# Kernel tuning notes

Hardware: AMD Instinct MI355X
Metric: run time of the kernel (lower is better)

The kernel has to match this reference:

```python
import jax, jax.numpy as jnp
import numpy as np

N = 50000      # nodes
E = 800000     # edges
F_IN = 128     # num_features
H = 64         # hidden_dim
G = 64         # graphs in batch
EPS = 1e-5


def setup_inputs() -> dict:
    ks = jax.random.split(jax.random.key(0), 16)
    x = jax.random.normal(ks[0], (N, F_IN), dtype=jnp.float32)
    edge_index = jax.random.randint(ks[1], (2, E), 0, N, dtype=jnp.int64)
    batch = jnp.sort(jax.random.randint(ks[2], (N,), 0, G, dtype=jnp.int64))
    s = 0.05
    inp = {"x": x, "edge_index": edge_index, "batch": batch}
    # GCNConv layers: W [out,in], bias [out]; BatchNorm gamma/beta [H]
    dims = [(H, F_IN), (H, H), (H, H)]
    for i, (o, ci) in enumerate(dims):
        inp[f"W{i}"] = jax.random.normal(ks[3 + i], (o, ci), dtype=jnp.float32) * s
        inp[f"b{i}"] = jnp.zeros((o,), dtype=jnp.float32)
        inp[f"g{i}"] = jnp.ones((o,), dtype=jnp.float32)
        inp[f"be{i}"] = jnp.zeros((o,), dtype=jnp.float32)
    inp["lin1_w"] = jax.random.normal(ks[10], (H // 2, H), dtype=jnp.float32) * s
    inp["lin1_b"] = jnp.zeros((H // 2,), dtype=jnp.float32)
    inp["lin2_w"] = jax.random.normal(ks[11], (1, H // 2), dtype=jnp.float32) * s
    inp["lin2_b"] = jnp.zeros((1,), dtype=jnp.float32)
    return inp


def _gcn_conv(x, src, dst, W, b):
    # PyG GCNConv: h = x W^T; add self-loops; symmetric deg^{-1/2} norm; scatter-add; + bias
    h = x @ W.T                                   # [N, out]
    n = x.shape[0]
    deg = jax.ops.segment_sum(jnp.ones(src.shape[0], h.dtype), dst, num_segments=n) + 1.0
    dinv = jax.lax.rsqrt(deg)                     # [N]
    msg = h[src] * (dinv[src] * dinv[dst])[:, None]   # per-edge messages
    agg = jax.ops.segment_sum(msg, dst, num_segments=n)
    agg = agg + h * (dinv * dinv)[:, None]        # self-loop contribution
    return agg + b


def _bn_relu(x, g, be):
    # BatchNorm1d (training-mode batch stats, biased var) + ReLU; dropout = identity (eval)
    m = x.mean(axis=0)
    v = jnp.var(x, axis=0)
    return jax.nn.relu((x - m) * jax.lax.rsqrt(v + EPS) * g + be)


def reference(x, edge_index, batch,
              W0, b0, g0, be0, W1, b1, g1, be1, W2, b2, g2, be2,
              lin1_w, lin1_b, lin2_w, lin2_b):
    src, dst = edge_index[0], edge_index[1]
    Ws = [(W0, b0, g0, be0), (W1, b1, g1, be1), (W2, b2, g2, be2)]
    h = x
    for (W, b, g, be) in Ws:
        h = _bn_relu(_gcn_conv(h, src, dst, W, b), g, be)
    # global mean pool over graphs
    sums = jax.ops.segment_sum(h, batch, num_segments=G)          # [G, H]
    cnt = jax.ops.segment_sum(jnp.ones((h.shape[0],), h.dtype), batch, num_segments=G)
    pooled = sums / jnp.maximum(cnt, 1.0)[:, None]
    h = jax.nn.relu(pooled @ lin1_w.T + lin1_b)
    return h @ lin2_w.T + lin2_b                                   # [G, 1]
```

## Files before the change

kernel.cpp:

```cpp
#include <hip/hip_runtime.h>

#define NN 50000
#define NE 800000
#define FIN 128
#define H 64
#define NG 64
#define BN_EPS 1e-5f
#define INV_N (1.0f / 50000.0f)
#define NBKT 196
#define PB 256
#define SLICE 64
#define BKCAP 8192
#define PROWS 16

__device__ __forceinline__ void f4acc(float4& a, const float4 b) {
    a.x += b.x; a.y += b.y; a.z += b.z; a.w += b.w;
}
__device__ __forceinline__ void f4accw(float4& a, const float4 b, float w) {
    a.x += b.x * w; a.y += b.y * w; a.z += b.z * w; a.w += b.w * w;
}

__global__ void prep(const float* __restrict__ W0, const float* __restrict__ W1,
                     const float* __restrict__ W2, const int* __restrict__ src,
                     const int* __restrict__ dst, float* __restrict__ Wt0,
                     float* __restrict__ Wt1, float* __restrict__ Wt2,
                     float* __restrict__ sl0, float* __restrict__ sl1,
                     float* __restrict__ sl2, float* __restrict__ pool,
                     float* __restrict__ cnt, int* __restrict__ done,
                     int* __restrict__ cnts, unsigned int* __restrict__ staged) {
    const int tid = threadIdx.x, bid = blockIdx.x;
    const int gtid = bid * 256 + tid;
    const int gsz = PB * 256;
    for (int i = gtid; i < 64 * 128; i += gsz) { sl0[i] = 0.f; sl1[i] = 0.f; sl2[i] = 0.f; }
    for (int i = gtid; i < NG * H; i += gsz) pool[i] = 0.f;
    if (gtid < NG) cnt[gtid] = 0.f;
    if (gtid == 0) *done = 0;
    for (int i = gtid; i < FIN * 64; i += gsz) {
        int k = i >> 6, o = i & 63;
        Wt0[i] = W0[o * FIN + k];
    }
    for (int i = gtid; i < H * 64; i += gsz) {
        int k = i >> 6, o = i & 63;
        Wt1[i] = W1[o * H + k];
        Wt2[i] = W2[o * H + k];
    }
    __shared__ int hcnt[NBKT];
    for (int i = tid; i < NBKT; i += 256) hcnt[i] = 0;
    __syncthreads();
    const int chunk = NE / PB;
    const int e0 = bid * chunk, e1 = e0 + chunk;
    for (int e = e0 + tid; e < e1; e += 256) {
        int d = dst[e];
        int s = src[e];
        int bkt = d >> 8;
        int idx = atomicAdd(&hcnt[bkt], 1);
        if (idx < SLICE)
            staged[(size_t)(bkt * PB + bid) * SLICE + idx] =
                (unsigned int)s | ((unsigned int)(d & 255) << 16);
    }
    __syncthreads();
    for (int i = tid; i < NBKT; i += 256) cnts[i * PB + bid] = min(hcnt[i], SLICE);
}

union CsrMmSh {
    struct { float Xs[64 * 68]; float Ws[64 * 64]; } mm;
    struct { int cnt[256]; int loc[256]; int cur[256]; int spre[257]; } csr;
};

__device__ __forceinline__ int slice_find(const int* __restrict__ spre, int t) {
    int lo = 0, hi = 255;
    while (lo < hi) {
        int mid = (lo + hi + 1) >> 1;
        if (spre[mid] <= t) lo = mid; else hi = mid - 1;
    }
    return lo;
}

template <int K>
__device__ __forceinline__ void mm_tile_body(int base, const float* __restrict__ x,
                                             const float* __restrict__ Wtg,
                                             const float* __restrict__ slots,
                                             const float* __restrict__ gamma,
                                             const float* __restrict__ beta,
                                             const float* __restrict__ dv,
                                             float* __restrict__ outp, float* Xs, float* Ws,
                                             float* st, int n) {
    const int tid = threadIdx.x;
    if (slots) {
        if (tid < 128) {
            float s0 = 0.f, s1 = 0.f, s2 = 0.f, s3 = 0.f;
            for (int k = 0; k < 64; k += 4) {
                s0 += slots[(k + 0) * 128 + tid];
                s1 += slots[(k + 1) * 128 + tid];
                s2 += slots[(k + 2) * 128 + tid];
                s3 += slots[(k + 3) * 128 + tid];
            }
            st[tid] = (s0 + s1) + (s2 + s3);
        }
        __syncthreads();
    }
    const int q = tid >> 4;
    const int co = (tid & 15) * 4;
    const int kq = (tid & 15) * 4;
    float4 a0 = make_float4(0.f, 0.f, 0.f, 0.f);
    float4 a1 = a0, a2 = a0, a3 = a0;

    for (int kc = 0; kc < K; kc += 64) {
        if (kc) __syncthreads();
        for (int i = tid; i < 64 * 64; i += 256) Ws[i] = Wtg[kc * 64 + i];
        {
            float4 sc = make_float4(1.f, 1.f, 1.f, 1.f);
            float4 sh = make_float4(0.f, 0.f, 0.f, 0.f);
            if (slots) {
                int kk = kc + kq;
                float4 s = *(const float4*)&st[kk];
                float4 ss = *(const float4*)&st[64 + kk];
                float4 gm = *(const float4*)&gamma[kk];
                float4 bt = *(const float4*)&beta[kk];
                float mx = s.x * INV_N, my = s.y * INV_N, mz = s.z * INV_N, mw = s.w * INV_N;
                sc.x = gm.x * rsqrtf(ss.x * INV_N - mx * mx + BN_EPS);
                sc.y = gm.y * rsqrtf(ss.y * INV_N - my * my + BN_EPS);
                sc.z = gm.z * rsqrtf(ss.z * INV_N - mz * mz + BN_EPS);
                sc.w = gm.w * rsqrtf(ss.w * INV_N - mw * mw + BN_EPS);
                sh.x = bt.x - mx * sc.x;
                sh.y = bt.y - my * sc.y;
                sh.z = bt.z - mz * sc.z;
                sh.w = bt.w - mw * sc.w;
            }
            for (int j = 0; j < 4; ++j) {
                int r = (tid >> 4) + j * 16;
                int row = base + r;
                float4 v = make_float4(0.f, 0.f, 0.f, 0.f);
                if (row < n) v = *(const float4*)&x[(size_t)row * K + kc + kq];
                if (slots) {
                    v.x = fmaxf(v.x * sc.x + sh.x, 0.f);
                    v.y = fmaxf(v.y * sc.y + sh.y, 0.f);
                    v.z = fmaxf(v.z * sc.z + sh.z, 0.f);
                    v.w = fmaxf(v.w * sc.w + sh.w, 0.f);
                }
                *(float4*)&Xs[r * 68 + kq] = v;
            }
        }
        __syncthreads();

#pragma unroll 2
        for (int k = 0; k < 64; k += 4) {
            float4 x0 = *(const float4*)&Xs[(q + 0) * 68 + k];
            float4 x1 = *(const float4*)&Xs[(q + 16) * 68 + k];
            float4 x2 = *(const float4*)&Xs[(q + 32) * 68 + k];
            float4 x3 = *(const float4*)&Xs[(q + 48) * 68 + k];
            float4 w0 = *(const float4*)&Ws[(k + 0) * 64 + co];
            float4 w1 = *(const float4*)&Ws[(k + 1) * 64 + co];
            float4 w2 = *(const float4*)&Ws[(k + 2) * 64 + co];
            float4 w3 = *(const float4*)&Ws[(k + 3) * 64 + co];

            a0.x += x0.x * w0.x + x0.y * w1.x + x0.z * w2.x + x0.w * w3.x;
            a0.y += x0.x * w0.y + x0.y * w1.y + x0.z * w2.y + x0.w * w3.y;
            a0.z += x0.x * w0.z + x0.y * w1.z + x0.z * w2.z + x0.w * w3.z;
            a0.w += x0.x * w0.w + x0.y * w1.w + x0.z * w2.w + x0.w * w3.w;

            a1.x += x1.x * w0.x + x1.y * w1.x + x1.z * w2.x + x1.w * w3.x;
            a1.y += x1.x * w0.y + x1.y * w1.y + x1.z * w2.y + x1.w * w3.y;
            a1.z += x1.x * w0.z + x1.y * w1.z + x1.z * w2.z + x1.w * w3.z;
            a1.w += x1.x * w0.w + x1.y * w1.w + x1.z * w2.w + x1.w * w3.w;

            a2.x += x2.x * w0.x + x2.y * w1.x + x2.z * w2.x + x2.w * w3.x;
            a2.y += x2.x * w0.y + x2.y * w1.y + x2.z * w2.y + x2.w * w3.y;
            a2.z += x2.x * w0.z + x2.y * w1.z + x2.z * w2.z + x2.w * w3.z;
            a2.w += x2.x * w0.w + x2.y * w1.w + x2.z * w2.w + x2.w * w3.w;

            a3.x += x3.x * w0.x + x3.y * w1.x + x3.z * w2.x + x3.w * w3.x;
            a3.y += x3.x * w0.y + x3.y * w1.y + x3.z * w2.y + x3.w * w3.y;
            a3.z += x3.x * w0.z + x3.y * w1.z + x3.z * w2.z + x3.w * w3.z;
            a3.w += x3.x * w0.w + x3.y * w1.w + x3.z * w2.w + x3.w * w3.w;
        }
    }

    int r0 = base + q;
    if (r0 < n) {
        float d = dv ? dv[r0] : 1.f;
        a0.x *= d; a0.y *= d; a0.z *= d; a0.w *= d;
        *(float4*)&outp[(size_t)r0 * H + co] = a0;
    }
    if (r0 + 16 < n) {
        float d = dv ? dv[r0 + 16] : 1.f;
        a1.x *= d; a1.y *= d; a1.z *= d; a1.w *= d;
        *(float4*)&outp[(size_t)(r0 + 16) * H + co] = a1;
    }
    if (r0 + 32 < n) {
        float d = dv ? dv[r0 + 32] : 1.f;
        a2.x *= d; a2.y *= d; a2.z *= d; a2.w *= d;
        *(float4*)&outp[(size_t)(r0 + 32) * H + co] = a2;
    }
    if (r0 + 48 < n) {
        float d = dv ? dv[r0 + 48] : 1.f;
        a3.x *= d; a3.y *= d; a3.z *= d; a3.w *= d;
        *(float4*)&outp[(size_t)(r0 + 48) * H + co] = a3;
    }
}

__global__ __launch_bounds__(256, 4) void csr_mm0(
    const unsigned int* __restrict__ staged, const int* __restrict__ cnts,
    int* __restrict__ rs, int* __restrict__ re, float* __restrict__ dinv,
    int* __restrict__ csr, const float* __restrict__ x, const float* __restrict__ Wt0,
    float* __restrict__ bufA) {
    __shared__ CsrMmSh sh;
    const int tid = threadIdx.x;
    if (blockIdx.x < NBKT) {
        const int b = blockIdx.x;
        int c = cnts[b * PB + tid];
        sh.csr.loc[tid] = c;
        sh.csr.cnt[tid] = 0;
        __syncthreads();
        for (int off = 1; off < 256; off <<= 1) {
            int t = (tid >= off) ? sh.csr.loc[tid - off] : 0;
            __syncthreads();
            sh.csr.loc[tid] += t;
            __syncthreads();
        }
        sh.csr.spre[tid] = sh.csr.loc[tid] - c;
        if (tid == 255) sh.csr.spre[256] = sh.csr.loc[255];
        __syncthreads();
        const int T = sh.csr.spre[256];
        for (int t = tid; t < T; t += 256) {
            int s = slice_find(sh.csr.spre, t);
            unsigned int u = staged[(size_t)(b * PB + s) * SLICE + (t - sh.csr.spre[s])];
            atomicAdd(&sh.csr.cnt[(u >> 16) & 255], 1);
        }
        __syncthreads();
        int v = sh.csr.cnt[tid];
        sh.csr.loc[tid] = v;
        __syncthreads();
        for (int off = 1; off < 256; off <<= 1) {
            int t = (tid >= off) ? sh.csr.loc[tid - off] : 0;
            __syncthreads();
            sh.csr.loc[tid] += t;
            __syncthreads();
        }
        const int start = b * BKCAP + sh.csr.loc[tid] - v;
        const int node = b * 256 + tid;
        if (node < NN) {
            rs[node] = start;
            re[node] = start + v;
            dinv[node] = rsqrtf((float)v + 1.0f);
        }
        sh.csr.cur[tid] = start;
        __syncthreads();
        for (int t = tid; t < T; t += 256) {
            int s = slice_find(sh.csr.spre, t);
            unsigned int u = staged[(size_t)(b * PB + s) * SLICE + (t - sh.csr.spre[s])];
            int j = atomicAdd(&sh.csr.cur[(u >> 16) & 255], 1);
            csr[j] = (int)(u & 0xFFFFu);
        }
    } else {
        mm_tile_body<FIN>((blockIdx.x - NBKT) * 64, x, Wt0, nullptr, nullptr, nullptr, nullptr,
                          bufA, sh.mm.Xs, sh.mm.Ws, nullptr, NN);
    }
}

__global__ __launch_bounds__(256, 4) void matmul_bn(const float* __restrict__ x,
                                                    const float* __restrict__ Wtg,
                                                    const float* __restrict__ slots,
                                                    const float* __restrict__ gamma,
                                                    const float* __restrict__ beta,
                                                    const float* __restrict__ dv,
                                                    float* __restrict__ outp, int n) {
    __shared__ float Xs[64 * 68];
    __shared__ float Ws[64 * 64];
    __shared__ __align__(16) float st[128];
    mm_tile_body<H>(blockIdx.x * 64, x, Wtg, slots, gamma, beta, dv, outp, Xs, Ws, st, n);
}

template <bool ED>
__global__ void gcn_gather(const float* __restrict__ h, const int* __restrict__ rs,
                           const int* __restrict__ re, const int* __restrict__ csrc,
                           const float* __restrict__ dv, const float* __restrict__ bias,
                           float* __restrict__ outp, float* __restrict__ slots, int n) {
    const int wv = threadIdx.x >> 6;
    const int lane = threadIdx.x & 63;
    const int e = lane >> 4;
    const int f4 = (lane & 15) * 4;
    const int d0 = blockIdx.x * 8 + wv * 2;
    float4 scc = make_float4(0.f, 0.f, 0.f, 0.f);
    float4 qcc = scc;
    if (d0 < n) {
        const int d1 = d0 + 1;
        const int rA = rs[d0];
        const int eA = re[d0];
        const int eB = re[d1];
        const float dA = dv[d0], dB = dv[d1];
        const float4 selfA = *(const float4*)&h[(size_t)d0 * H + f4];
        const float4 selfB = *(const float4*)&h[(size_t)d1 * H + f4];
        const float4 bq = *(const float4*)&bias[f4];
        float4 a0 = make_float4(0.f, 0.f, 0.f, 0.f), a1 = a0, b0 = a0, b1 = a0;
        int jA = rA + e;
        int jB = eA + e;
        while (jA + 4 < eA && jB + 4 < eB) {
            int sA0 = csrc[jA], sA1 = csrc[jA + 4];
            int sB0 = csrc[jB], sB1 = csrc[jB + 4];
            float wA0 = ED ? dv[sA0] : 1.f, wA1 = ED ? dv[sA1] : 1.f;
            float wB0 = ED ? dv[sB0] : 1.f, wB1 = ED ? dv[sB1] : 1.f;
            f4accw(a0, *(const float4*)&h[(size_t)sA0 * H + f4], wA0);
            f4accw(a1, *(const float4*)&h[(size_t)sA1 * H + f4], wA1);
            f4accw(b0, *(const float4*)&h[(size_t)sB0 * H + f4], wB0);
            f4accw(b1, *(const float4*)&h[(size_t)sB1 * H + f4], wB1);
            jA += 8;
            jB += 8;
        }
        while (jA + 4 < eA) {
            int s0 = csrc[jA], s1 = csrc[jA + 4];
            float w0 = ED ? dv[s0] : 1.f, w1 = ED ? dv[s1] : 1.f;
            f4accw(a0, *(const float4*)&h[(size_t)s0 * H + f4], w0);
            f4accw(a1, *(const float4*)&h[(size_t)s1 * H + f4], w1);
            jA += 8;
        }
        if (jA < eA) {
            int s = csrc[jA];
            f4accw(a0, *(const float4*)&h[(size_t)s * H + f4], ED ? dv[s] : 1.f);
        }
        while (jB + 4 < eB) {
            int s0 = csrc[jB], s1 = csrc[jB + 4];
            float w0 = ED ? dv[s0] : 1.f, w1 = ED ? dv[s1] : 1.f;
            f4accw(b0, *(const float4*)&h[(size_t)s0 * H + f4], w0);
            f4accw(b1, *(const float4*)&h[(size_t)s1 * H + f4], w1);
            jB += 8;
        }
        if (jB < eB) {
            int s = csrc[jB];
            f4accw(b0, *(const float4*)&h[(size_t)s * H + f4], ED ? dv[s] : 1.f);
        }
        f4acc(a0, a1);
        f4acc(b0, b1);
        a0.x += __shfl_xor(a0.x, 16); a0.x += __shfl_xor(a0.x, 32);
        a0.y += __shfl_xor(a0.y, 16); a0.y += __shfl_xor(a0.y, 32);
        a0.z += __shfl_xor(a0.z, 16); a0.z += __shfl_xor(a0.z, 32);
        a0.w += __shfl_xor(a0.w, 16); a0.w += __shfl_xor(a0.w, 32);
        b0.x += __shfl_xor(b0.x, 16); b0.x += __shfl_xor(b0.x, 32);
        b0.y += __shfl_xor(b0.y, 16); b0.y += __shfl_xor(b0.y, 32);
        b0.z += __shfl_xor(b0.z, 16); b0.z += __shfl_xor(b0.z, 32);
        b0.w += __shfl_xor(b0.w, 16); b0.w += __shfl_xor(b0.w, 32);
        const float sfA = ED ? dA : 1.f;
        const float sfB = ED ? dB : 1.f;
        float4 vA, vB;
        vA.x = bq.x + dA * (a0.x + sfA * selfA.x);
        vA.y = bq.y + dA * (a0.y + sfA * selfA.y);
        vA.z = bq.z + dA * (a0.z + sfA * selfA.z);
        vA.w = bq.w + dA * (a0.w + sfA * selfA.w);
        vB.x = bq.x + dB * (b0.x + sfB * selfB.x);
        vB.y = bq.y + dB * (b0.y + sfB * selfB.y);
        vB.z = bq.z + dB * (b0.z + sfB * selfB.z);
        vB.w = bq.w + dB * (b0.w + sfB * selfB.w);
        if (e < 2) {
            float4 vS;
            vS.x = e ? vB.x : vA.x;
            vS.y = e ? vB.y : vA.y;
            vS.z = e ? vB.z : vA.z;
            vS.w = e ? vB.w : vA.w;
            *(float4*)&outp[(size_t)(d0 + e) * H + f4] = vS;
        }
        scc.x = vA.x + vB.x; scc.y = vA.y + vB.y;
        scc.z = vA.z + vB.z; scc.w = vA.w + vB.w;
        qcc.x = vA.x * vA.x + vB.x * vB.x;
        qcc.y = vA.y * vA.y + vB.y * vB.y;
        qcc.z = vA.z * vA.z + vB.z * vB.z;
        qcc.w = vA.w * vA.w + vB.w * vB.w;
    }
    __shared__ float4 reds[64], redq[64];
    if (e == 0) {
        reds[wv * 16 + (lane & 15)] = scc;
        redq[wv * 16 + (lane & 15)] = qcc;
    }
    __syncthreads();
    const int tid = threadIdx.x;
    if (tid < 32) {
        const int t = tid & 15;
        const float4* rp = (tid < 16) ? reds : redq;
        float4 r0 = rp[t], r1 = rp[16 + t], r2 = rp[32 + t], r3 = rp[48 + t];
        float4 s;
        s.x = (r0.x + r1.x) + (r2.x + r3.x);
        s.y = (r0.y + r1.y) + (r2.y + r3.y);
        s.z = (r0.z + r1.z) + (r2.z + r3.z);
        s.w = (r0.w + r1.w) + (r2.w + r3.w);
        float* slot = slots + (blockIdx.x & 63) * 128 + (tid < 16 ? 0 : 64) + t * 4;
        atomicAdd(&slot[0], s.x);
        atomicAdd(&slot[1], s.y);
        atomicAdd(&slot[2], s.z);
        atomicAdd(&slot[3], s.w);
    }
}

__global__ void pool_mlp(const float* __restrict__ h, const float* __restrict__ slots,
                         const float* __restrict__ gamma, const float* __restrict__ beta,
                         const int* __restrict__ batch, float* __restrict__ pool,
                         float* __restrict__ cnt, int* __restrict__ done,
                         const float* __restrict__ l1w, const float* __restrict__ l1b,
                         const float* __restrict__ l2w, const float* __restrict__ l2b,
                         float* __restrict__ out, int n) {
    __shared__ __align__(16) float pst[128];
    __shared__ int ticket;
    const int tid = threadIdx.x;
    if (tid < 128) {
        float s0 = 0.f, s1 = 0.f, s2 = 0.f, s3 = 0.f;
        for (int k = 0; k < 64; k += 4) {
            s0 += slots[(k + 0) * 128 + tid];
            s1 += slots[(k + 1) * 128 + tid];
            s2 += slots[(k + 2) * 128 + tid];
            s3 += slots[(k + 3) * 128 + tid];
        }
        pst[tid] = (s0 + s1) + (s2 + s3);
    }
    __syncthreads();
    const int wv = tid >> 6;
    const int c = tid & 63;
    const float mean = pst[c] * INV_N;
    const float var = pst[64 + c] * INV_N - mean * mean;
    const float scv = gamma[c] * rsqrtf(var + BN_EPS);
    const float shv = beta[c] - mean * scv;
    const int r0 = (blockIdx.x * 4 + wv) * PROWS;
    if (r0 < n) {
        const int r1 = min(r0 + PROWS, n);
        int cur = batch[r0];
        float acc = 0.f;
        int nl = 0;
        for (int r = r0; r < r1; ++r) {
            int gg = batch[r];
            if (gg != cur) {
                atomicAdd(&pool[cur * H + c], acc);
                if (c == 0) atomicAdd(&cnt[cur], (float)nl);
                cur = gg;
                acc = 0.f;
                nl = 0;
            }
            acc += fmaxf(h[(size_t)r * H + c] * scv + shv, 0.f);
            ++nl;
        }
        atomicAdd(&pool[cur * H + c], acc);
        if (c == 0) atomicAdd(&cnt[cur], (float)nl);
    }
    __threadfence();
    __syncthreads();
    if (tid == 0) ticket = atomicAdd(done, 1);
    __syncthreads();
    if (ticket == (int)gridDim.x - 1) {
        for (int gb = 0; gb < NG; gb += 8) {
            int g = gb + (tid >> 5);
            int j = tid & 31;
            float inv = 1.0f / fmaxf(cnt[g], 1.0f);
            float s = l1b[j];
            for (int k = 0; k < H; ++k) s += pool[g * H + k] * inv * l1w[j * H + k];
            float v = fmaxf(s, 0.0f) * l2w[j];
            for (int off = 16; off > 0; off >>= 1) v += __shfl_down(v, off, 32);
            if (j == 0) out[g] = v + l2b[0];
        }
    }
}

extern "C" void kernel_launch(void* const* d_in, const int* in_sizes, int n_in,
                              void* d_out, int out_size, void* d_ws, size_t ws_size,
                              hipStream_t stream) {
    const float* x = (const float*)d_in[0];
    const int* ei = (const int*)d_in[1];
    const int* batch = (const int*)d_in[2];
    const float* W[3] = {(const float*)d_in[3], (const float*)d_in[7], (const float*)d_in[11]};
    const float* b[3] = {(const float*)d_in[4], (const float*)d_in[8], (const float*)d_in[12]};
    const float* g[3] = {(const float*)d_in[5], (const float*)d_in[9], (const float*)d_in[13]};
    const float* be[3] = {(const float*)d_in[6], (const float*)d_in[10], (const float*)d_in[14]};
    const float* l1w = (const float*)d_in[15];
    const float* l1b = (const float*)d_in[16];
    const float* l2w = (const float*)d_in[17];
    const float* l2b = (const float*)d_in[18];
    float* out = (float*)d_out;

    const int* src = ei;
    const int* dst = ei + NE;

    char* wsb = (char*)d_ws;
    size_t off = 0;
    auto alloc = [&](size_t elems) {
        void* p = wsb + off;
        off += elems * 4;
        return p;
    };
    float* dinv = (float*)alloc(50048);
    float* bufA = (float*)alloc((size_t)NN * H);
    float* bufB = (float*)alloc((size_t)NN * H);
    float* slots[3] = {(float*)alloc(64 * 128), (float*)alloc(64 * 128), (float*)alloc(64 * 128)};
    float* pool = (float*)alloc(NG * H);
    float* cnt = (float*)alloc(64);
    int* done = (int*)alloc(64);
    float* Wt[3] = {(float*)alloc(FIN * 64), (float*)alloc(H * 64), (float*)alloc(H * 64)};
    int* rs = (int*)alloc(50048);
    int* re = (int*)alloc(50048);
    int* cnts = (int*)alloc((size_t)NBKT * PB);
    unsigned int* staged = (unsigned int*)alloc((size_t)NBKT * PB * SLICE);
    int* csr = (int*)alloc((size_t)NBKT * BKCAP);

    const int grid_mm = (NN + 63) / 64;
    const int grid_gather = (NN + 7) / 8;

    prep<<<PB, 256, 0, stream>>>(W[0], W[1], W[2], src, dst, Wt[0], Wt[1], Wt[2], slots[0],
                                 slots[1], slots[2], pool, cnt, done, cnts, staged);
    csr_mm0<<<NBKT + grid_mm, 256, 0, stream>>>(staged, cnts, rs, re, dinv, csr, x, Wt[0], bufA);
    gcn_gather<true><<<grid_gather, 256, 0, stream>>>(bufA, rs, re, csr, dinv, b[0], bufB,
                                                      slots[0], NN);
    matmul_bn<<<grid_mm, 256, 0, stream>>>(bufB, Wt[1], slots[0], g[0], be[0], dinv, bufA, NN);
    gcn_gather<false><<<grid_gather, 256, 0, stream>>>(bufA, rs, re, csr, dinv, b[1], bufB,
                                                       slots[1], NN);
    matmul_bn<<<grid_mm, 256, 0, stream>>>(bufB, Wt[2], slots[1], g[1], be[1], dinv, bufA, NN);
    gcn_gather<false><<<grid_gather, 256, 0, stream>>>(bufA, rs, re, csr, dinv, b[2], bufB,
                                                       slots[2], NN);
    const int pool_grid = ((NN + PROWS - 1) / PROWS + 3) / 4;
    pool_mlp<<<pool_grid, 256, 0, stream>>>(bufB, slots[2], g[2], be[2], batch, pool, cnt, done,
                                            l1w, l1b, l2w, l2b, out, NN);
}
```

Measured before the change: 379.2 us.

## Split hidden features into 16-wide segments and gather one segment per launch

Hidden activations are stored in a segmented layout of four contiguous [N,16] slabs instead of row-major [N,64]. Each GCN gather then runs as four launches, one per segment, so its random neighbor reads touch a 3.2MB slab that can stay cache-resident. Matmul and pool kernels are adapted to the new layout, and the last-block ticket for the MLP is replaced by a separate final kernel. The cost is that the CSR indices and degree weights are re-read four times per layer, plus extra launches and 64-byte scattered reads.

```diff
diff --git a/kernel.cpp b/kernel.cpp
--- a/kernel.cpp
+++ b/kernel.cpp
@@ -12,6 +12,7 @@
 #define SLICE 64
 #define BKCAP 8192
 #define PROWS 16
+#define NSEG 4
 
 __device__ __forceinline__ void f4acc(float4& a, const float4 b) {
     a.x += b.x; a.y += b.y; a.z += b.z; a.w += b.w;
@@ -26,15 +27,14 @@
                      float* __restrict__ Wt1, float* __restrict__ Wt2,
                      float* __restrict__ sl0, float* __restrict__ sl1,
                      float* __restrict__ sl2, float* __restrict__ pool,
-                     float* __restrict__ cnt, int* __restrict__ done,
-                     int* __restrict__ cnts, unsigned int* __restrict__ staged) {
+                     float* __restrict__ cnt, int* __restrict__ cnts,
+                     unsigned int* __restrict__ staged) {
     const int tid = threadIdx.x, bid = blockIdx.x;
     const int gtid = bid * 256 + tid;
     const int gsz = PB * 256;
     for (int i = gtid; i < 64 * 128; i += gsz) { sl0[i] = 0.f; sl1[i] = 0.f; sl2[i] = 0.f; }
     for (int i = gtid; i < NG * H; i += gsz) pool[i] = 0.f;
     if (gtid < NG) cnt[gtid] = 0.f;
-    if (gtid == 0) *done = 0;
     for (int i = gtid; i < FIN * 64; i += gsz) {
         int k = i >> 6, o = i & 63;
         Wt0[i] = W0[o * FIN + k];
@@ -76,7 +76,7 @@
     return lo;
 }
 
-template <int K>
+template <int K, bool SEGIN>
 __device__ __forceinline__ void mm_tile_body(int base, const float* __restrict__ x,
                                              const float* __restrict__ Wtg,
                                              const float* __restrict__ slots,
@@ -109,14 +109,14 @@
         if (kc) __syncthreads();
         for (int i = tid; i < 64 * 64; i += 256) Ws[i] = Wtg[kc * 64 + i];
         {
+            const int kidx = kc + kq;
             float4 sc = make_float4(1.f, 1.f, 1.f, 1.f);
             float4 sh = make_float4(0.f, 0.f, 0.f, 0.f);
             if (slots) {
-                int kk = kc + kq;
-                float4 s = *(const float4*)&st[kk];
-                float4 ss = *(const float4*)&st[64 + kk];
-                float4 gm = *(const float4*)&gamma[kk];
-                float4 bt = *(const float4*)&beta[kk];
+                float4 s = *(const float4*)&st[kidx];
+                float4 ss = *(const float4*)&st[64 + kidx];
+                float4 gm = *(const float4*)&gamma[kidx];
+                float4 bt = *(const float4*)&beta[kidx];
                 float mx = s.x * INV_N, my = s.y * INV_N, mz = s.z * INV_N, mw = s.w * INV_N;
                 sc.x = gm.x * rsqrtf(ss.x * INV_N - mx * mx + BN_EPS);
                 sc.y = gm.y * rsqrtf(ss.y * INV_N - my * my + BN_EPS);
@@ -131,7 +131,12 @@
                 int r = (tid >> 4) + j * 16;
                 int row = base + r;
                 float4 v = make_float4(0.f, 0.f, 0.f, 0.f);
-                if (row < n) v = *(const float4*)&x[(size_t)row * K + kc + kq];
+                if (row < n) {
+                    if (SEGIN)
+                        v = *(const float4*)&x[((size_t)(kidx >> 4) * NN + row) * 16 + (kidx & 15)];
+                    else
+                        v = *(const float4*)&x[(size_t)row * K + kidx];
+                }
                 if (slots) {
                     v.x = fmaxf(v.x * sc.x + sh.x, 0.f);
                     v.y = fmaxf(v.y * sc.y + sh.y, 0.f);
@@ -176,26 +181,27 @@
         }
     }
 
+    const int sg = co >> 4, so = co & 15;
     int r0 = base + q;
     if (r0 < n) {
         float d = dv ? dv[r0] : 1.f;
         a0.x *= d; a0.y *= d; a0.z *= d; a0.w *= d;
-        *(float4*)&outp[(size_t)r0 * H + co] = a0;
+        *(float4*)&outp[((size_t)sg * NN + r0) * 16 + so] = a0;
     }
     if (r0 + 16 < n) {
         float d = dv ? dv[r0 + 16] : 1.f;
         a1.x *= d; a1.y *= d; a1.z *= d; a1.w *= d;
-        *(float4*)&outp[(size_t)(r0 + 16) * H + co] = a1;
+        *(float4*)&outp[((size_t)sg * NN + r0 + 16) * 16 + so] = a1;
     }
     if (r0 + 32 < n) {
         float d = dv ? dv[r0 + 32] : 1.f;
         a2.x *= d; a2.y *= d; a2.z *= d; a2.w *= d;
-        *(float4*)&outp[(size_t)(r0 + 32) * H + co] = a2;
+        *(float4*)&outp[((size_t)sg * NN + r0 + 32) * 16 + so] = a2;
     }
     if (r0 + 48 < n) {
         float d = dv ? dv[r0 + 48] : 1.f;
         a3.x *= d; a3.y *= d; a3.z *= d; a3.w *= d;
-        *(float4*)&outp[(size_t)(r0 + 48) * H + co] = a3;
+        *(float4*)&outp[((size_t)sg * NN + r0 + 48) * 16 + so] = a3;
     }
 }
 
@@ -253,8 +259,8 @@
             csr[j] = (int)(u & 0xFFFFu);
         }
     } else {
-        mm_tile_body<FIN>((blockIdx.x - NBKT) * 64, x, Wt0, nullptr, nullptr, nullptr, nullptr,
-                          bufA, sh.mm.Xs, sh.mm.Ws, nullptr, NN);
+        mm_tile_body<FIN, false>((blockIdx.x - NBKT) * 64, x, Wt0, nullptr, nullptr, nullptr,
+                                 nullptr, bufA, sh.mm.Xs, sh.mm.Ws, nullptr, NN);
     }
 }
 
@@ -268,120 +274,76 @@
     __shared__ float Xs[64 * 68];
     __shared__ float Ws[64 * 64];
     __shared__ __align__(16) float st[128];
-    mm_tile_body<H>(blockIdx.x * 64, x, Wtg, slots, gamma, beta, dv, outp, Xs, Ws, st, n);
+    mm_tile_body<H, true>(blockIdx.x * 64, x, Wtg, slots, gamma, beta, dv, outp, Xs, Ws, st, n);
 }
 
 template <bool ED>
-__global__ void gcn_gather(const float* __restrict__ h, const int* __restrict__ rs,
-                           const int* __restrict__ re, const int* __restrict__ csrc,
-                           const float* __restrict__ dv, const float* __restrict__ bias,
-                           float* __restrict__ outp, float* __restrict__ slots, int n) {
-    const int wv = threadIdx.x >> 6;
-    const int lane = threadIdx.x & 63;
-    const int e = lane >> 4;
-    const int f4 = (lane & 15) * 4;
-    const int d0 = blockIdx.x * 8 + wv * 2;
-    float4 scc = make_float4(0.f, 0.f, 0.f, 0.f);
-    float4 qcc = scc;
-    if (d0 < n) {
-        const int d1 = d0 + 1;
-        const int rA = rs[d0];
-        const int eA = re[d0];
-        const int eB = re[d1];
-        const float dA = dv[d0], dB = dv[d1];
-        const float4 selfA = *(const float4*)&h[(size_t)d0 * H + f4];
-        const float4 selfB = *(const float4*)&h[(size_t)d1 * H + f4];
-        const float4 bq = *(const float4*)&bias[f4];
-        float4 a0 = make_float4(0.f, 0.f, 0.f, 0.f), a1 = a0, b0 = a0, b1 = a0;
-        int jA = rA + e;
-        int jB = eA + e;
-        while (jA + 4 < eA && jB + 4 < eB) {
-            int sA0 = csrc[jA], sA1 = csrc[jA + 4];
-            int sB0 = csrc[jB], sB1 = csrc[jB + 4];
-            float wA0 = ED ? dv[sA0] : 1.f, wA1 = ED ? dv[sA1] : 1.f;
-            float wB0 = ED ? dv[sB0] : 1.f, wB1 = ED ? dv[sB1] : 1.f;
-            f4accw(a0, *(const float4*)&h[(size_t)sA0 * H + f4], wA0);
-            f4accw(a1, *(const float4*)&h[(size_t)sA1 * H + f4], wA1);
-            f4accw(b0, *(const float4*)&h[(size_t)sB0 * H + f4], wB0);
-            f4accw(b1, *(const float4*)&h[(size_t)sB1 * H + f4], wB1);
-            jA += 8;
-            jB += 8;
-        }
-        while (jA + 4 < eA) {
-            int s0 = csrc[jA], s1 = csrc[jA + 4];
-            float w0 = ED ? dv[s0] : 1.f, w1 = ED ? dv[s1] : 1.f;
-            f4accw(a0, *(const float4*)&h[(size_t)s0 * H + f4], w0);
-            f4accw(a1, *(const float4*)&h[(size_t)s1 * H + f4], w1);
-            jA += 8;
-        }
-        if (jA < eA) {
-            int s = csrc[jA];
-            f4accw(a0, *(const float4*)&h[(size_t)s * H + f4], ED ? dv[s] : 1.f);
-        }
-        while (jB + 4 < eB) {
-            int s0 = csrc[jB], s1 = csrc[jB + 4];
-            float w0 = ED ? dv[s0] : 1.f, w1 = ED ? dv[s1] : 1.f;
-            f4accw(b0, *(const float4*)&h[(size_t)s0 * H + f4], w0);
-            f4accw(b1, *(const float4*)&h[(size_t)s1 * H + f4], w1);
-            jB += 8;
-        }
-        if (jB < eB) {
-            int s = csrc[jB];
-            f4accw(b0, *(const float4*)&h[(size_t)s * H + f4], ED ? dv[s] : 1.f);
-        }
-        f4acc(a0, a1);
-        f4acc(b0, b1);
-        a0.x += __shfl_xor(a0.x, 16); a0.x += __shfl_xor(a0.x, 32);
-        a0.y += __shfl_xor(a0.y, 16); a0.y += __shfl_xor(a0.y, 32);
-        a0.z += __shfl_xor(a0.z, 16); a0.z += __shfl_xor(a0.z, 32);
-        a0.w += __shfl_xor(a0.w, 16); a0.w += __shfl_xor(a0.w, 32);
-        b0.x += __shfl_xor(b0.x, 16); b0.x += __shfl_xor(b0.x, 32);
-        b0.y += __shfl_xor(b0.y, 16); b0.y += __shfl_xor(b0.y, 32);
-        b0.z += __shfl_xor(b0.z, 16); b0.z += __shfl_xor(b0.z, 32);
-        b0.w += __shfl_xor(b0.w, 16); b0.w += __shfl_xor(b0.w, 32);
-        const float sfA = ED ? dA : 1.f;
-        const float sfB = ED ? dB : 1.f;
-        float4 vA, vB;
-        vA.x = bq.x + dA * (a0.x + sfA * selfA.x);
-        vA.y = bq.y + dA * (a0.y + sfA * selfA.y);
-        vA.z = bq.z + dA * (a0.z + sfA * selfA.z);
-        vA.w = bq.w + dA * (a0.w + sfA * selfA.w);
-        vB.x = bq.x + dB * (b0.x + sfB * selfB.x);
-        vB.y = bq.y + dB * (b0.y + sfB * selfB.y);
-        vB.z = bq.z + dB * (b0.z + sfB * selfB.z);
-        vB.w = bq.w + dB * (b0.w + sfB * selfB.w);
-        if (e < 2) {
-            float4 vS;
-            vS.x = e ? vB.x : vA.x;
-            vS.y = e ? vB.y : vA.y;
-            vS.z = e ? vB.z : vA.z;
-            vS.w = e ? vB.w : vA.w;
-            *(float4*)&outp[(size_t)(d0 + e) * H + f4] = vS;
-        }
-        scc.x = vA.x + vB.x; scc.y = vA.y + vB.y;
-        scc.z = vA.z + vB.z; scc.w = vA.w + vB.w;
-        qcc.x = vA.x * vA.x + vB.x * vB.x;
-        qcc.y = vA.y * vA.y + vB.y * vB.y;
-        qcc.z = vA.z * vA.z + vB.z * vB.z;
-        qcc.w = vA.w * vA.w + vB.w * vB.w;
-    }
-    __shared__ float4 reds[64], redq[64];
-    if (e == 0) {
-        reds[wv * 16 + (lane & 15)] = scc;
-        redq[wv * 16 + (lane & 15)] = qcc;
+__global__ __launch_bounds__(256) void gather_seg(const float* __restrict__ h,
+                                                  const int* __restrict__ rs,
+                                                  const int* __restrict__ re,
+                                                  const int* __restrict__ csrc,
+                                                  const float* __restrict__ dv,
+                                                  const float* __restrict__ bias,
+                                                  float* __restrict__ outp,
+                                                  float* __restrict__ slots, int seg) {
+    const int tid = threadIdx.x;
+    const int wv = tid >> 6;
+    const int lane = tid & 63;
+    const int fl = lane & 3;
+    const int ss = (lane >> 2) & 3;
+    const int ds = lane >> 4;
+    const int d = (blockIdx.x * 4 + wv) * 4 + ds;
+    const float* hseg = h + (size_t)seg * NN * 16;
+    const int fo = fl * 4;
+    const int j1 = re[d];
+    const float dA = dv[d];
+    float4 acc = make_float4(0.f, 0.f, 0.f, 0.f);
+    int j = rs[d] + ss;
+    while (j + 4 < j1) {
+        int s0 = csrc[j], s1 = csrc[j + 4];
+        if (ED) {
+            f4accw(acc, *(const float4*)&hseg[(size_t)s0 * 16 + fo], dv[s0]);
+            f4accw(acc, *(const float4*)&hseg[(size_t)s1 * 16 + fo], dv[s1]);
+        } else {
+            f4acc(acc, *(const float4*)&hseg[(size_t)s0 * 16 + fo]);
+            f4acc(acc, *(const float4*)&hseg[(size_t)s1 * 16 + fo]);
+        }
+        j += 8;
+    }
+    if (j < j1) {
+        int s0 = csrc[j];
+        if (ED)
+            f4accw(acc, *(const float4*)&hseg[(size_t)s0 * 16 + fo], dv[s0]);
+        else
+            f4acc(acc, *(const float4*)&hseg[(size_t)s0 * 16 + fo]);
+    }
+    acc.x += __shfl_xor(acc.x, 4); acc.x += __shfl_xor(acc.x, 8);
+    acc.y += __shfl_xor(acc.y, 4); acc.y += __shfl_xor(acc.y, 8);
+    acc.z += __shfl_xor(acc.z, 4); acc.z += __shfl_xor(acc.z, 8);
+    acc.w += __shfl_xor(acc.w, 4); acc.w += __shfl_xor(acc.w, 8);
+    const float4 self = *(const float4*)&hseg[(size_t)d * 16 + fo];
+    const float4 bq = *(const float4*)&bias[seg * 16 + fo];
+    const float sf = ED ? dA : 1.f;
+    float4 v;
+    v.x = bq.x + dA * (acc.x + sf * self.x);
+    v.y = bq.y + dA * (acc.y + sf * self.y);
+    v.z = bq.z + dA * (acc.z + sf * self.z);
+    v.w = bq.w + dA * (acc.w + sf * self.w);
+    if (ss == 0) *(float4*)&outp[((size_t)seg * NN + d) * 16 + fo] = v;
+    __shared__ float4 red[2][4][4][4];
+    if (ss == 0) {
+        float4 vq;
+        vq.x = v.x * v.x; vq.y = v.y * v.y; vq.z = v.z * v.z; vq.w = v.w * v.w;
+        red[0][wv][ds][fl] = v;
+        red[1][wv][ds][fl] = vq;
     }
     __syncthreads();
-    const int tid = threadIdx.x;
-    if (tid < 32) {
-        const int t = tid & 15;
-        const float4* rp = (tid < 16) ? reds : redq;
-        float4 r0 = rp[t], r1 = rp[16 + t], r2 = rp[32 + t], r3 = rp[48 + t];
-        float4 s;
-        s.x = (r0.x + r1.x) + (r2.x + r3.x);
-        s.y = (r0.y + r1.y) + (r2.y + r3.y);
-        s.z = (r0.z + r1.z) + (r2.z + r3.z);
-        s.w = (r0.w + r1.w) + (r2.w + r3.w);
-        float* slot = slots + (blockIdx.x & 63) * 128 + (tid < 16 ? 0 : 64) + t * 4;
+    if (tid < 8) {
+        int a = tid >> 2, f2 = tid & 3;
+        float4 s = make_float4(0.f, 0.f, 0.f, 0.f);
+#pragma unroll
+        for (int i = 0; i < 16; ++i) f4acc(s, red[a][i >> 2][i & 3][f2]);
+        float* slot = slots + (blockIdx.x & 63) * 128 + a * 64 + seg * 16 + f2 * 4;
         atomicAdd(&slot[0], s.x);
         atomicAdd(&slot[1], s.y);
         atomicAdd(&slot[2], s.z);
@@ -389,70 +351,65 @@
     }
 }
 
-__global__ void pool_mlp(const float* __restrict__ h, const float* __restrict__ slots,
+__global__ void pool_seg(const float* __restrict__ h, const float* __restrict__ slots,
                          const float* __restrict__ gamma, const float* __restrict__ beta,
                          const int* __restrict__ batch, float* __restrict__ pool,
-                         float* __restrict__ cnt, int* __restrict__ done,
-                         const float* __restrict__ l1w, const float* __restrict__ l1b,
-                         const float* __restrict__ l2w, const float* __restrict__ l2b,
-                         float* __restrict__ out, int n) {
+                         float* __restrict__ cnt, int n) {
     __shared__ __align__(16) float pst[128];
-    __shared__ int ticket;
-    const int tid = threadIdx.x;
-    if (tid < 128) {
+    if (threadIdx.x < 128) {
         float s0 = 0.f, s1 = 0.f, s2 = 0.f, s3 = 0.f;
         for (int k = 0; k < 64; k += 4) {
-            s0 += slots[(k + 0) * 128 + tid];
-            s1 += slots[(k + 1) * 128 + tid];
-            s2 += slots[(k + 2) * 128 + tid];
-            s3 += slots[(k + 3) * 128 + tid];
-        }
-        pst[tid] = (s0 + s1) + (s2 + s3);
+            s0 += slots[(k + 0) * 128 + threadIdx.x];
+            s1 += slots[(k + 1) * 128 + threadIdx.x];
+            s2 += slots[(k + 2) * 128 + threadIdx.x];
+            s3 += slots[(k + 3) * 128 + threadIdx.x];
+        }
+        pst[threadIdx.x] = (s0 + s1) + (s2 + s3);
     }
     __syncthreads();
-    const int wv = tid >> 6;
-    const int c = tid & 63;
-    const float mean = pst[c] * INV_N;
-    const float var = pst[64 + c] * INV_N - mean * mean;
-    const float scv = gamma[c] * rsqrtf(var + BN_EPS);
-    const float shv = beta[c] - mean * scv;
-    const int r0 = (blockIdx.x * 4 + wv) * PROWS;
-    if (r0 < n) {
-        const int r1 = min(r0 + PROWS, n);
-        int cur = batch[r0];
-        float acc = 0.f;
-        int nl = 0;
-        for (int r = r0; r < r1; ++r) {
-            int gg = batch[r];
-            if (gg != cur) {
-                atomicAdd(&pool[cur * H + c], acc);
-                if (c == 0) atomicAdd(&cnt[cur], (float)nl);
-                cur = gg;
-                acc = 0.f;
-                nl = 0;
-            }
-            acc += fmaxf(h[(size_t)r * H + c] * scv + shv, 0.f);
-            ++nl;
-        }
-        atomicAdd(&pool[cur * H + c], acc);
-        if (c == 0) atomicAdd(&cnt[cur], (float)nl);
-    }
-    __threadfence();
-    __syncthreads();
-    if (tid == 0) ticket = atomicAdd(done, 1);
-    __syncthreads();
-    if (ticket == (int)gridDim.x - 1) {
-        for (int gb = 0; gb < NG; gb += 8) {
-            int g = gb + (tid >> 5);
-            int j = tid & 31;
-            float inv = 1.0f / fmaxf(cnt[g], 1.0f);
-            float s = l1b[j];
-            for (int k = 0; k < H; ++k) s += pool[g * H + k] * inv * l1w[j * H + k];
-            float v = fmaxf(s, 0.0f) * l2w[j];
-            for (int off = 16; off > 0; off >>= 1) v += __shfl_down(v, off, 32);
-            if (j == 0) out[g] = v + l2b[0];
-        }
-    }
+    int wave = blockIdx.x * 4 + (threadIdx.x >> 6);
+    int c = threadIdx.x & 63;
+    int r0 = wave * PROWS;
+    if (r0 >= n) return;
+    int r1 = min(r0 + PROWS, n);
+    float mean = pst[c] * INV_N;
+    float var = pst[64 + c] * INV_N - mean * mean;
+    float sc = gamma[c] * rsqrtf(var + BN_EPS);
+    float sh = beta[c] - mean * sc;
+    const size_t segbase = (size_t)(c >> 4) * NN * 16 + (c & 15);
+    int cur = batch[r0];
+    float acc = 0.f;
+    int nlocal = 0;
+    for (int r = r0; r < r1; ++r) {
+        int g = batch[r];
+        if (g != cur) {
+            atomicAdd(&pool[cur * H + c], acc);
+            if (c == 0) atomicAdd(&cnt[cur], (float)nlocal);
+            cur = g;
+            acc = 0.f;
+            nlocal = 0;
+        }
+        acc += fmaxf(h[segbase + (size_t)r * 16] * sc + sh, 0.f);
+        ++nlocal;
+    }
+    atomicAdd(&pool[cur * H + c], acc);
+    if (c == 0) atomicAdd(&cnt[cur], (float)nlocal);
+}
+
+__global__ void final_mlp(const float* __restrict__ pool, const float* __restrict__ cnt,
+                          const float* __restrict__ l1w, const float* __restrict__ l1b,
+                          const float* __restrict__ l2w, const float* __restrict__ l2b,
+                          float* __restrict__ out) {
+    int tid = blockIdx.x * 256 + threadIdx.x;
+    int g = tid >> 5;
+    int j = tid & 31;
+    if (g >= NG) return;
+    float inv = 1.0f / fmaxf(cnt[g], 1.0f);
+    float s = l1b[j];
+    for (int k = 0; k < H; ++k) s += pool[g * H + k] * inv * l1w[j * H + k];
+    float v = fmaxf(s, 0.0f) * l2w[j];
+    for (int off = 16; off > 0; off >>= 1) v += __shfl_down(v, off, 32);
+    if (j == 0) out[g] = v + l2b[0];
 }
 
 extern "C" void kernel_launch(void* const* d_in, const int* in_sizes, int n_in,
@@ -487,7 +444,6 @@
     float* slots[3] = {(float*)alloc(64 * 128), (float*)alloc(64 * 128), (float*)alloc(64 * 128)};
     float* pool = (float*)alloc(NG * H);
     float* cnt = (float*)alloc(64);
-    int* done = (int*)alloc(64);
     float* Wt[3] = {(float*)alloc(FIN * 64), (float*)alloc(H * 64), (float*)alloc(H * 64)};
     int* rs = (int*)alloc(50048);
     int* re = (int*)alloc(50048);
@@ -496,20 +452,23 @@
     int* csr = (int*)alloc((size_t)NBKT * BKCAP);
 
     const int grid_mm = (NN + 63) / 64;
-    const int grid_gather = (NN + 7) / 8;
+    const int grid_gs = NN / 16;
 
     prep<<<PB, 256, 0, stream>>>(W[0], W[1], W[2], src, dst, Wt[0], Wt[1], Wt[2], slots[0],
-                                 slots[1], slots[2], pool, cnt, done, cnts, staged);
+                                 slots[1], slots[2], pool, cnt, cnts, staged);
     csr_mm0<<<NBKT + grid_mm, 256, 0, stream>>>(staged, cnts, rs, re, dinv, csr, x, Wt[0], bufA);
-    gcn_gather<true><<<grid_gather, 256, 0, stream>>>(bufA, rs, re, csr, dinv, b[0], bufB,
-                                                      slots[0], NN);
+    for (int s = 0; s < NSEG; ++s)
+        gather_seg<true><<<grid_gs, 256, 0, stream>>>(bufA, rs, re, csr, dinv, b[0], bufB,
+                                                      slots[0], s);
     matmul_bn<<<grid_mm, 256, 0, stream>>>(bufB, Wt[1], slots[0], g[0], be[0], dinv, bufA, NN);
-    gcn_gather<false><<<grid_gather, 256, 0, stream>>>(bufA, rs, re, csr, dinv, b[1], bufB,
-                                                       slots[1], NN);
+    for (int s = 0; s < NSEG; ++s)
+        gather_seg<false><<<grid_gs, 256, 0, stream>>>(bufA, rs, re, csr, dinv, b[1], bufB,
+                                                       slots[1], s);
     matmul_bn<<<grid_mm, 256, 0, stream>>>(bufB, Wt[2], slots[1], g[1], be[1], dinv, bufA, NN);
-    gcn_gather<false><<<grid_gather, 256, 0, stream>>>(bufA, rs, re, csr, dinv, b[2], bufB,
-                                                       slots[2], NN);
+    for (int s = 0; s < NSEG; ++s)
+        gather_seg<false><<<grid_gs, 256, 0, stream>>>(bufA, rs, re, csr, dinv, b[2], bufB,
+                                                       slots[2], s);
     const int pool_grid = ((NN + PROWS - 1) / PROWS + 3) / 4;
-    pool_mlp<<<pool_grid, 256, 0, stream>>>(bufB, slots[2], g[2], be[2], batch, pool, cnt, done,
-                                            l1w, l1b, l2w, l2b, out, NN);
-}
+    pool_seg<<<pool_grid, 256, 0, stream>>>(bufB, slots[2], g[2], be[2], batch, pool, cnt, NN);
+    final_mlp<<<8, 256, 0, stream>>>(pool, cnt, l1w, l1b, l2w, l2b, out);
+}
```

New measurement: 366.6 us. 1.03x faster.
